# Optimization experiments

Measured on AMD Instinct MI355X. Metric: run time of the kernel, lower is better.

Reference implementation:

```python
import jax, jax.numpy as jnp
import numpy as np
import math

D_MODEL = 512
N_HEADS = 8
WINDOW = 64
LN_EPS = 1e-5


def _layernorm(x, g, b):
    mu = jnp.mean(x, axis=-1, keepdims=True)
    var = jnp.var(x, axis=-1, keepdims=True)
    return (x - mu) * jax.lax.rsqrt(var + LN_EPS) * g + b


def setup_inputs() -> dict:
    key = jax.random.key(0)
    ks = jax.random.split(key, 8)
    B, L, D = 4, 2048, D_MODEL
    s = 0.02
    return {
        "x": jax.random.normal(ks[0], (B, L, D), jnp.float32),
        "wq": jax.random.normal(ks[1], (D, D), jnp.float32) * s,
        "bq": jnp.zeros((D,), jnp.float32),
        "wk": jax.random.normal(ks[2], (D, D), jnp.float32) * s,
        "bk": jnp.zeros((D,), jnp.float32),
        "wv": jax.random.normal(ks[3], (D, D), jnp.float32) * s,
        "bv": jnp.zeros((D,), jnp.float32),
        "wo": jax.random.normal(ks[4], (D, D), jnp.float32) * s,
        "bo": jnp.zeros((D,), jnp.float32),
        "ln1_g": jnp.ones((D,), jnp.float32),
        "ln1_b": jnp.zeros((D,), jnp.float32),
        "w1": jax.random.normal(ks[5], (D, 4 * D), jnp.float32) * s,
        "b1": jnp.zeros((4 * D,), jnp.float32),
        "w2": jax.random.normal(ks[6], (4 * D, D), jnp.float32) * s,
        "b2": jnp.zeros((D,), jnp.float32),
        "ln2_g": jnp.ones((D,), jnp.float32),
        "ln2_b": jnp.zeros((D,), jnp.float32),
    }


def reference(x, wq, bq, wk, bk, wv, bv, wo, bo, ln1_g, ln1_b, w1, b1, w2, b2, ln2_g, ln2_b):
    B, L, D = x.shape
    H, dk = N_HEADS, D // N_HEADS
    # QKV projections -> [B, H, L, dk]
    q = (x @ wq + bq).reshape(B, L, H, dk).transpose(0, 2, 1, 3)
    k = (x @ wk + bk).reshape(B, L, H, dk).transpose(0, 2, 1, 3)
    v = (x @ wv + bv).reshape(B, L, H, dk).transpose(0, 2, 1, 3)
    # dense scores with sliding-window band mask |i-j| <= WINDOW (faithful to original)
    idx = jnp.arange(L)
    band = jnp.abs(idx[:, None] - idx[None, :]) <= WINDOW  # [L, L] bool
    scores = jnp.einsum("bhid,bhjd->bhij", q, k) / math.sqrt(dk)
    scores = jnp.where(band, scores, -jnp.inf)
    attn = jax.nn.softmax(scores, axis=-1)
    out = jnp.einsum("bhij,bhjd->bhid", attn, v)  # [B, H, L, dk]
    out = out.transpose(0, 2, 1, 3).reshape(B, L, D)
    attn_out = out @ wo + bo
    h = _layernorm(x + attn_out, ln1_g, ln1_b)
    ff = jax.nn.relu(h @ w1 + b1) @ w2 + b2
    return _layernorm(h + ff, ln2_g, ln2_b)
```

## Files before the change

### kernel.cpp

```cpp
#include <hip/hip_runtime.h>
#include <hip/hip_bf16.h>

#define D_MODEL 512
#define NHEADS 8
#define DK 64
#define WIN 64
#define SEQ 2048
#define BATCH 4
#define ROWS (BATCH*SEQ)

typedef unsigned short u16;
using bf16x8 = __attribute__((ext_vector_type(8))) short;
using f32x4  = __attribute__((ext_vector_type(4))) float;
using u16x4  = __attribute__((ext_vector_type(4))) unsigned short;

__device__ __forceinline__ u16 f2b(float f) {
  union { float f; unsigned u; } v; v.f = f;
  unsigned r = v.u + 0x7FFFu + ((v.u >> 16) & 1u);
  return (u16)(r >> 16);
}
__device__ __forceinline__ float b2f(u16 h) {
  union { unsigned u; float f; } v; v.u = ((unsigned)h) << 16; return v.f;
}

__device__ __forceinline__ void gload16(const u16* g, u16* l) {
  __builtin_amdgcn_global_load_lds((const __attribute__((address_space(1))) void*)g,
                                   (__attribute__((address_space(3))) void*)l, 16, 0, 0);
}

__global__ __launch_bounds__(256)
void prep_kernel(const float* __restrict__ wq, const float* __restrict__ wk,
                 const float* __restrict__ wv, const float* __restrict__ wo,
                 const float* __restrict__ w1, const float* __restrict__ w2,
                 const float* __restrict__ x,
                 u16* __restrict__ wqt, u16* __restrict__ wkt, u16* __restrict__ wvt,
                 u16* __restrict__ wot, u16* __restrict__ w1t, u16* __restrict__ w2t,
                 u16* __restrict__ xb)
{
  __shared__ u16 T[64][72];
  const int t = blockIdx.x;
  const float* src; u16* dst; int K, N, lt; bool tr = true;
  if (t < 256)      { int m = t >> 6; lt = t & 63;
                      src = m==0?wq:(m==1?wk:(m==2?wv:wo));
                      dst = m==0?wqt:(m==1?wkt:(m==2?wvt:wot));
                      K = 512; N = 512; }
  else if (t < 512) { src = w1; dst = w1t; K = 512;  N = 2048; lt = t-256; }
  else if (t < 768) { src = w2; dst = w2t; K = 2048; N = 512;  lt = t-512; }
  else              { src = x;  dst = xb;  K = 8192; N = 512;  lt = t-768; tr = false; }
  const int ntj = N >> 6;
  const int ti = lt / ntj, tj = lt - ti*ntj;
  const int tid = threadIdx.x;
  const int r = tid >> 2, c0 = (tid & 3) << 4;

  const float* sp = src + (size_t)(ti*64 + r)*N + tj*64 + c0;
  u16 h[16];
  #pragma unroll
  for (int u = 0; u < 4; ++u) {
    float4 v = *(const float4*)(sp + u*4);
    h[u*4+0]=f2b(v.x); h[u*4+1]=f2b(v.y); h[u*4+2]=f2b(v.z); h[u*4+3]=f2b(v.w);
  }
  if (!tr) {
    u16* dp = dst + (size_t)(ti*64 + r)*N + tj*64 + c0;
    *(bf16x8*)(dp)     = *(bf16x8*)&h[0];
    *(bf16x8*)(dp + 8) = *(bf16x8*)&h[8];
    return;
  }
  #pragma unroll
  for (int u = 0; u < 16; ++u) T[r][c0+u] = h[u];
  __syncthreads();
  u16 o[16];
  #pragma unroll
  for (int u = 0; u < 16; ++u) o[u] = T[c0+u][r];
  u16* dp = dst + (size_t)(tj*64 + r)*K + ti*64 + c0;
  *(bf16x8*)(dp)     = *(bf16x8*)&o[0];
  *(bf16x8*)(dp + 8) = *(bf16x8*)&o[8];
}

__device__ __forceinline__ void mainloop_bt(
    const u16* __restrict__ A, const u16* __restrict__ Bt, int K,
    int m0, int n0, int tid, f32x4 (&acc)[4][4], u16* Asl, u16* Bsl)
{
  const int lane = tid & 63, wave = tid >> 6;
  const int wr = wave >> 1, wc = wave & 1;
  const int l15 = lane & 15, lq = lane >> 4;
  const int ar = lane >> 2;
  const int ac = (lane & 3) << 3;

  const u16* ag0 = A  + (size_t)(m0 + wave*32 + ar)*K + ac;
  const u16* bg0 = Bt + (size_t)(n0 + wave*32 + ar)*K + ac;
  u16* const aslw = Asl + wave*1024;
  u16* const bslw = Bsl + wave*1024;

  for (int k0 = 0; k0 < K; k0 += 32) {
    __syncthreads();
    gload16(ag0 + k0,          aslw);
    gload16(ag0 + k0 + 16*K,   aslw + 512);
    gload16(bg0 + k0,          bslw);
    gload16(bg0 + k0 + 16*K,   bslw + 512);
    __syncthreads();

    bf16x8 af[4], bfr[4];
    #pragma unroll
    for (int m = 0; m < 4; ++m)
      af[m] = *(const bf16x8*)(&Asl[(wr*64 + m*16 + l15)*32 + lq*8]);
    #pragma unroll
    for (int n = 0; n < 4; ++n)
      bfr[n] = *(const bf16x8*)(&Bsl[(wc*64 + n*16 + l15)*32 + lq*8]);
    #pragma unroll
    for (int m = 0; m < 4; ++m)
      #pragma unroll
      for (int n = 0; n < 4; ++n)
        acc[m][n] = __builtin_amdgcn_mfma_f32_16x16x32_bf16(af[m], bfr[n], acc[m][n], 0, 0, 0);
  }
}

__global__ __launch_bounds__(256)
void qkv_kernel(const u16* __restrict__ xb,
                const u16* __restrict__ wqt, const float* __restrict__ bq,
                const u16* __restrict__ wkt, const float* __restrict__ bk,
                const u16* __restrict__ wvt, const float* __restrict__ bv,
                u16* __restrict__ qo, u16* __restrict__ ko, u16* __restrict__ vo)
{
  __shared__ __align__(16) u16 Asl[128*32];
  __shared__ __align__(16) u16 Bsl[128*32];
  const u16* Wt; const float* bias; u16* out;
  if (blockIdx.z == 0)      { Wt = wqt; bias = bq; out = qo; }
  else if (blockIdx.z == 1) { Wt = wkt; bias = bk; out = ko; }
  else                      { Wt = wvt; bias = bv; out = vo; }

  const int tid = threadIdx.x;
  const int lane = tid & 63, wave = tid >> 6;
  const int wr = wave >> 1, wc = wave & 1;
  const int l15 = lane & 15, lq = lane >> 4;
  const int m0 = blockIdx.y * 128, n0 = blockIdx.x * 128;

  f32x4 acc[4][4] = {};
  mainloop_bt(xb, Wt, 512, m0, n0, tid, acc, Asl, Bsl);

  #pragma unroll
  for (int n = 0; n < 4; ++n) {
    const int col = n0 + wc*64 + n*16 + l15;
    const float bv2 = bias[col];
    const int h = col >> 6, d = col & 63;
    #pragma unroll
    for (int m = 0; m < 4; ++m)
      #pragma unroll
      for (int j = 0; j < 4; ++j) {
        const int row = m0 + wr*64 + m*16 + lq*4 + j;
        const int b = row >> 11, l = row & (SEQ-1);
        out[(((size_t)(b*NHEADS + h))*SEQ + l)*DK + d] = f2b(acc[m][n][j] + bv2);
      }
  }
}

#define EP_RES  1
#define EP_RELU 2

template<int EP>
__global__ __launch_bounds__(256)
void gemm_bt(const u16* __restrict__ A, const u16* __restrict__ Bt,
             const float* __restrict__ bias, const float* __restrict__ resid,
             void* __restrict__ out_, int K, int N)
{
  __shared__ __align__(16) u16 Asl[128*32];
  __shared__ __align__(16) u16 Bsl[128*32];

  const int tid = threadIdx.x;
  const int lane = tid & 63, wave = tid >> 6;
  const int wr = wave >> 1, wc = wave & 1;
  const int l15 = lane & 15, lq = lane >> 4;
  const int m0 = blockIdx.y * 128, n0 = blockIdx.x * 128;

  f32x4 acc[4][4] = {};
  mainloop_bt(A, Bt, K, m0, n0, tid, acc, Asl, Bsl);

  #pragma unroll
  for (int n = 0; n < 4; ++n) {
    const int col = n0 + wc*64 + n*16 + l15;
    const float bv2 = bias[col];
    #pragma unroll
    for (int m = 0; m < 4; ++m)
      #pragma unroll
      for (int j = 0; j < 4; ++j) {
        const int row = m0 + wr*64 + m*16 + lq*4 + j;
        const size_t o = (size_t)row*N + col;
        float val = acc[m][n][j] + bv2;
        if (EP == EP_RES)  ((float*)out_)[o] = val + resid[o];
        else               ((u16*)out_)[o]   = f2b(fmaxf(val, 0.0f));
      }
  }
}

__global__ __launch_bounds__(256)
void attn_kernel(const u16* __restrict__ q, const u16* __restrict__ k,
                 const u16* __restrict__ v, u16* __restrict__ ctx)
{
  __shared__ __align__(16) u16 Ksl[192*40];
  __shared__ __align__(16) u16 Vt[64*200];
  __shared__ __align__(16) u16 Pl[4][16*200];

  const int bid = blockIdx.x;
  const int t = bid & 31, h = (bid >> 5) & 7, b = bid >> 8;
  const int qs = t*64;
  const int ks0 = max(0, qs - WIN);
  const int ks1 = min(SEQ, qs + 64 + WIN);
  const int span = ks1 - ks0;

  const size_t hoff = ((size_t)(b*NHEADS + h))*SEQ*DK;
  const u16* kh = k + hoff;
  const u16* vh = v + hoff;
  const int tid = threadIdx.x;

  #pragma unroll
  for (int i = 0; i < 6; ++i) {
    int e = tid + i*256;
    int r = e >> 3, c8 = (e & 7) << 3;
    bf16x8 val = {};
    if (r < span) val = *(const bf16x8*)(kh + (size_t)(ks0+r)*DK + c8);
    *(bf16x8*)(&Ksl[r*40 + c8]) = val;
  }
  #pragma unroll
  for (int i = 0; i < 12; ++i) {
    int e = tid + i*256;
    int j = e >> 4, d4 = (e & 15) << 2;
    u16x4 val{};
    if (j < span) val = *(const u16x4*)(vh + (size_t)(ks0+j)*DK + d4);
    #pragma unroll
    for (int u = 0; u < 4; ++u) {
      int d = d4 + u;
      int col = ((((j >> 3) ^ ((d >> 2) & 7)) << 3) | (j & 7));
      Vt[d*200 + col] = (u16)val[u];
    }
  }
  __syncthreads();

  const int wave = tid >> 6, lane = tid & 63;
  const int lq = lane >> 4, l15 = lane & 15;

  const u16* qrow = q + hoff + (size_t)(qs + wave*16 + l15)*DK;
  const bf16x8 qf0 = *(const bf16x8*)(qrow + lq*8);
  const bf16x8 qf1 = *(const bf16x8*)(qrow + 32 + lq*8);

  f32x4 sacc[12];
  #pragma unroll
  for (int m = 0; m < 12; ++m) sacc[m] = f32x4{0.f,0.f,0.f,0.f};
  #pragma unroll
  for (int m = 0; m < 12; ++m) {
    const u16* kr = &Ksl[(m*16 + l15)*40];
    bf16x8 ka0 = *(const bf16x8*)(kr + lq*8);
    bf16x8 ka1 = *(const bf16x8*)(kr + 32 + lq*8);
    sacc[m] = __builtin_amdgcn_mfma_f32_16x16x32_bf16(ka0, qf0, sacc[m], 0, 0, 0);
    sacc[m] = __builtin_amdgcn_mfma_f32_16x16x32_bf16(ka1, qf1, sacc[m], 0, 0, 0);
  }

  const int ig = qs + wave*16 + l15;
  float mx = -3.0e38f;
  #pragma unroll
  for (int m = 0; m < 12; ++m)
    #pragma unroll
    for (int r = 0; r < 4; ++r) {
      int jg = ks0 + m*16 + lq*4 + r;
      bool ok = (jg < ks1) && (jg >= ig - WIN) && (jg <= ig + WIN);
      float sv = ok ? sacc[m][r]*0.125f : -3.0e38f;
      sacc[m][r] = sv;
      mx = fmaxf(mx, sv);
    }
  mx = fmaxf(mx, __shfl_xor(mx, 16));
  mx = fmaxf(mx, __shfl_xor(mx, 32));
  float sum = 0.f;
  #pragma unroll
  for (int m = 0; m < 12; ++m)
    #pragma unroll
    for (int r = 0; r < 4; ++r) {
      float p = __expf(sacc[m][r] - mx);
      sacc[m][r] = p;
      sum += p;
    }
  sum += __shfl_xor(sum, 16);
  sum += __shfl_xor(sum, 32);
  const float inv = 1.0f / sum;

  u16* pw = &Pl[wave][0];
  #pragma unroll
  for (int m = 0; m < 12; ++m) {
    unsigned lo = (unsigned)f2b(sacc[m][0]*inv) | ((unsigned)f2b(sacc[m][1]*inv) << 16);
    unsigned hi = (unsigned)f2b(sacc[m][2]*inv) | ((unsigned)f2b(sacc[m][3]*inv) << 16);
    uint2 pk = make_uint2(lo, hi);
    *(uint2*)(&pw[l15*200 + m*16 + lq*4]) = pk;
  }

  f32x4 oacc[4] = {};
  #pragma unroll
  for (int kst = 0; kst < 6; ++kst) {
    bf16x8 pa = *(const bf16x8*)(&pw[l15*200 + kst*32 + lq*8]);
    #pragma unroll
    for (int n = 0; n < 4; ++n) {
      int d = n*16 + l15;
      int col = (((kst*4 + lq) ^ ((d >> 2) & 7)) << 3);
      bf16x8 vb = *(const bf16x8*)(&Vt[d*200 + col]);
      oacc[n] = __builtin_amdgcn_mfma_f32_16x16x32_bf16(pa, vb, oacc[n], 0, 0, 0);
    }
  }

  #pragma unroll
  for (int n = 0; n < 4; ++n)
    #pragma unroll
    for (int r = 0; r < 4; ++r) {
      int i = wave*16 + lq*4 + r;
      ctx[((size_t)b*SEQ + qs + i)*D_MODEL + h*DK + n*16 + l15] = f2b(oacc[n][r]);
    }
}

template<bool WB16>
__global__ __launch_bounds__(256)
void ln_kernel(const float* __restrict__ in, const float* __restrict__ g,
               const float* __restrict__ bb, float* __restrict__ out,
               u16* __restrict__ out16)
{
  const int row = blockIdx.x*4 + (threadIdx.x >> 6);
  const int lane = threadIdx.x & 63;
  const float* p = in + (size_t)row*D_MODEL + lane*8;
  float4 v0 = *(const float4*)(p);
  float4 v1 = *(const float4*)(p + 4);
  float s  = v0.x+v0.y+v0.z+v0.w + v1.x+v1.y+v1.z+v1.w;
  float sq = v0.x*v0.x+v0.y*v0.y+v0.z*v0.z+v0.w*v0.w
           + v1.x*v1.x+v1.y*v1.y+v1.z*v1.z+v1.w*v1.w;
  #pragma unroll
  for (int off = 32; off; off >>= 1) { s += __shfl_xor(s, off); sq += __shfl_xor(sq, off); }
  const float mean = s * (1.0f/D_MODEL);
  const float var  = sq * (1.0f/D_MODEL) - mean*mean;
  const float rstd = rsqrtf(var + 1e-5f);
  float4 g0 = *(const float4*)(g + lane*8);
  float4 g1 = *(const float4*)(g + lane*8 + 4);
  float4 b0 = *(const float4*)(bb + lane*8);
  float4 b1 = *(const float4*)(bb + lane*8 + 4);
  float4 o0, o1;
  o0.x = (v0.x-mean)*rstd*g0.x + b0.x;
  o0.y = (v0.y-mean)*rstd*g0.y + b0.y;
  o0.z = (v0.z-mean)*rstd*g0.z + b0.z;
  o0.w = (v0.w-mean)*rstd*g0.w + b0.w;
  o1.x = (v1.x-mean)*rstd*g1.x + b1.x;
  o1.y = (v1.y-mean)*rstd*g1.y + b1.y;
  o1.z = (v1.z-mean)*rstd*g1.z + b1.z;
  o1.w = (v1.w-mean)*rstd*g1.w + b1.w;
  float* qo = out + (size_t)row*D_MODEL + lane*8;
  *(float4*)(qo)     = o0;
  *(float4*)(qo + 4) = o1;
  if (WB16) {
    u16 hh[8];
    hh[0]=f2b(o0.x); hh[1]=f2b(o0.y); hh[2]=f2b(o0.z); hh[3]=f2b(o0.w);
    hh[4]=f2b(o1.x); hh[5]=f2b(o1.y); hh[6]=f2b(o1.z); hh[7]=f2b(o1.w);
    *(bf16x8*)(out16 + (size_t)row*D_MODEL + lane*8) = *(bf16x8*)&hh[0];
  }
}

extern "C" void kernel_launch(void* const* d_in, const int* in_sizes, int n_in,
                              void* d_out, int out_size, void* d_ws, size_t ws_size,
                              hipStream_t stream)
{
  (void)in_sizes; (void)n_in; (void)out_size; (void)ws_size;
  const float* x  = (const float*)d_in[0];
  const float* wq = (const float*)d_in[1];
  const float* bq = (const float*)d_in[2];
  const float* wk = (const float*)d_in[3];
  const float* bk = (const float*)d_in[4];
  const float* wv = (const float*)d_in[5];
  const float* bv = (const float*)d_in[6];
  const float* wo = (const float*)d_in[7];
  const float* bo = (const float*)d_in[8];
  const float* g1 = (const float*)d_in[9];
  const float* be1= (const float*)d_in[10];
  const float* w1 = (const float*)d_in[11];
  const float* b1 = (const float*)d_in[12];
  const float* w2 = (const float*)d_in[13];
  const float* b2 = (const float*)d_in[14];
  const float* g2 = (const float*)d_in[15];
  const float* be2= (const float*)d_in[16];

  const size_t RD = (size_t)ROWS * D_MODEL;
  u16* W = (u16*)d_ws;
  u16*   xb   = W;
  u16*   qb   = W + RD;
  u16*   kb   = W + 2*RD;
  u16*   vb   = W + 3*RD;
  u16*   ctxb = W + 4*RD;
  u16*   hb16 = W + 5*RD;
  float* hbuf = (float*)(W + 6*RD);
  u16*   wqt  = W + 8*RD;
  u16*   wkt  = wqt + 512*512;
  u16*   wvt  = wkt + 512*512;
  u16*   wot  = wvt + 512*512;
  u16*   w1t  = wot + 512*512;
  u16*   w2t  = w1t + 512*2048;
  u16*   ff1  = qb;
  float* pre  = (float*)d_out;
  float* outp = (float*)d_out;

  dim3 blk(256);
  prep_kernel<<<dim3(1792), blk, 0, stream>>>(wq, wk, wv, wo, w1, w2, x,
                                              wqt, wkt, wvt, wot, w1t, w2t, xb);
  qkv_kernel<<<dim3(4,64,3), blk, 0, stream>>>(xb, wqt, bq, wkt, bk, wvt, bv, qb, kb, vb);
  attn_kernel<<<dim3(BATCH*NHEADS*32), blk, 0, stream>>>(qb, kb, vb, ctxb);
  gemm_bt<EP_RES><<<dim3(4,64), blk, 0, stream>>>(ctxb, wot, bo, x, pre, 512, 512);
  ln_kernel<true><<<dim3(ROWS/4), blk, 0, stream>>>(pre, g1, be1, hbuf, hb16);
  gemm_bt<EP_RELU><<<dim3(16,64), blk, 0, stream>>>(hb16, w1t, b1, nullptr, ff1, 512, 2048);
  gemm_bt<EP_RES><<<dim3(4,64), blk, 0, stream>>>(ff1, w2t, b2, hbuf, pre, 2048, 512);
  ln_kernel<false><<<dim3(ROWS/4), blk, 0, stream>>>(pre, g2, be2, outp, nullptr);
}
```

Baseline: 268.3 us.

## Double-buffer LDS in GEMM mainloop and swap grid axes for M-major launch

The GEMM mainloop now uses two LDS buffers. The next K-tile's global-to-LDS loads are issued before the current tile's MFMAs, and only one barrier per iteration remains instead of two. Separately, grid x now indexes M tiles and y indexes N tiles, which changes block scheduling order and therefore L2 reuse of weight and activation tiles. LDS use per block doubles to 32KB, which could reduce occupancy.

```diff
diff --git a/kernel.cpp b/kernel.cpp
--- a/kernel.cpp
+++ b/kernel.cpp
@@ -78,7 +78,8 @@
 
 __device__ __forceinline__ void mainloop_bt(
     const u16* __restrict__ A, const u16* __restrict__ Bt, int K,
-    int m0, int n0, int tid, f32x4 (&acc)[4][4], u16* Asl, u16* Bsl)
+    int m0, int n0, int tid, f32x4 (&acc)[4][4],
+    u16 (*Asl)[128*32], u16 (*Bsl)[128*32])
 {
   const int lane = tid & 63, wave = tid >> 6;
   const int wr = wave >> 1, wc = wave & 1;
@@ -88,30 +89,41 @@
 
   const u16* ag0 = A  + (size_t)(m0 + wave*32 + ar)*K + ac;
   const u16* bg0 = Bt + (size_t)(n0 + wave*32 + ar)*K + ac;
-  u16* const aslw = Asl + wave*1024;
-  u16* const bslw = Bsl + wave*1024;
-
-  for (int k0 = 0; k0 < K; k0 += 32) {
-    __syncthreads();
-    gload16(ag0 + k0,          aslw);
-    gload16(ag0 + k0 + 16*K,   aslw + 512);
-    gload16(bg0 + k0,          bslw);
-    gload16(bg0 + k0 + 16*K,   bslw + 512);
-    __syncthreads();
-
+
+  auto stage = [&](int buf, int k0) {
+    u16* aslw = &Asl[buf][wave*1024];
+    u16* bslw = &Bsl[buf][wave*1024];
+    gload16(ag0 + k0,        aslw);
+    gload16(ag0 + k0 + 16*K, aslw + 512);
+    gload16(bg0 + k0,        bslw);
+    gload16(bg0 + k0 + 16*K, bslw + 512);
+  };
+  auto compute = [&](int buf) {
     bf16x8 af[4], bfr[4];
     #pragma unroll
     for (int m = 0; m < 4; ++m)
-      af[m] = *(const bf16x8*)(&Asl[(wr*64 + m*16 + l15)*32 + lq*8]);
+      af[m] = *(const bf16x8*)(&Asl[buf][(wr*64 + m*16 + l15)*32 + lq*8]);
     #pragma unroll
     for (int n = 0; n < 4; ++n)
-      bfr[n] = *(const bf16x8*)(&Bsl[(wc*64 + n*16 + l15)*32 + lq*8]);
+      bfr[n] = *(const bf16x8*)(&Bsl[buf][(wc*64 + n*16 + l15)*32 + lq*8]);
     #pragma unroll
     for (int m = 0; m < 4; ++m)
       #pragma unroll
       for (int n = 0; n < 4; ++n)
         acc[m][n] = __builtin_amdgcn_mfma_f32_16x16x32_bf16(af[m], bfr[n], acc[m][n], 0, 0, 0);
-  }
+  };
+
+  stage(0, 0);
+  __syncthreads();
+  int cur = 0;
+  const int nt = K >> 5;
+  for (int t = 0; t < nt - 1; ++t) {
+    stage(cur ^ 1, (t + 1) << 5);
+    compute(cur);
+    __syncthreads();
+    cur ^= 1;
+  }
+  compute(cur);
 }
 
 __global__ __launch_bounds__(256)
@@ -121,8 +133,8 @@
                 const u16* __restrict__ wvt, const float* __restrict__ bv,
                 u16* __restrict__ qo, u16* __restrict__ ko, u16* __restrict__ vo)
 {
-  __shared__ __align__(16) u16 Asl[128*32];
-  __shared__ __align__(16) u16 Bsl[128*32];
+  __shared__ __align__(16) u16 Asl[2][128*32];
+  __shared__ __align__(16) u16 Bsl[2][128*32];
   const u16* Wt; const float* bias; u16* out;
   if (blockIdx.z == 0)      { Wt = wqt; bias = bq; out = qo; }
   else if (blockIdx.z == 1) { Wt = wkt; bias = bk; out = ko; }
@@ -132,7 +144,7 @@
   const int lane = tid & 63, wave = tid >> 6;
   const int wr = wave >> 1, wc = wave & 1;
   const int l15 = lane & 15, lq = lane >> 4;
-  const int m0 = blockIdx.y * 128, n0 = blockIdx.x * 128;
+  const int m0 = blockIdx.x * 128, n0 = blockIdx.y * 128;
 
   f32x4 acc[4][4] = {};
   mainloop_bt(xb, Wt, 512, m0, n0, tid, acc, Asl, Bsl);
@@ -162,14 +174,14 @@
              const float* __restrict__ bias, const float* __restrict__ resid,
              void* __restrict__ out_, int K, int N)
 {
-  __shared__ __align__(16) u16 Asl[128*32];
-  __shared__ __align__(16) u16 Bsl[128*32];
+  __shared__ __align__(16) u16 Asl[2][128*32];
+  __shared__ __align__(16) u16 Bsl[2][128*32];
 
   const int tid = threadIdx.x;
   const int lane = tid & 63, wave = tid >> 6;
   const int wr = wave >> 1, wc = wave & 1;
   const int l15 = lane & 15, lq = lane >> 4;
-  const int m0 = blockIdx.y * 128, n0 = blockIdx.x * 128;
+  const int m0 = blockIdx.x * 128, n0 = blockIdx.y * 128;
 
   f32x4 acc[4][4] = {};
   mainloop_bt(A, Bt, K, m0, n0, tid, acc, Asl, Bsl);
@@ -399,11 +411,11 @@
   dim3 blk(256);
   prep_kernel<<<dim3(1792), blk, 0, stream>>>(wq, wk, wv, wo, w1, w2, x,
                                               wqt, wkt, wvt, wot, w1t, w2t, xb);
-  qkv_kernel<<<dim3(4,64,3), blk, 0, stream>>>(xb, wqt, bq, wkt, bk, wvt, bv, qb, kb, vb);
+  qkv_kernel<<<dim3(64,4,3), blk, 0, stream>>>(xb, wqt, bq, wkt, bk, wvt, bv, qb, kb, vb);
   attn_kernel<<<dim3(BATCH*NHEADS*32), blk, 0, stream>>>(qb, kb, vb, ctxb);
-  gemm_bt<EP_RES><<<dim3(4,64), blk, 0, stream>>>(ctxb, wot, bo, x, pre, 512, 512);
+  gemm_bt<EP_RES><<<dim3(64,4), blk, 0, stream>>>(ctxb, wot, bo, x, pre, 512, 512);
   ln_kernel<true><<<dim3(ROWS/4), blk, 0, stream>>>(pre, g1, be1, hbuf, hb16);
-  gemm_bt<EP_RELU><<<dim3(16,64), blk, 0, stream>>>(hb16, w1t, b1, nullptr, ff1, 512, 2048);
-  gemm_bt<EP_RES><<<dim3(4,64), blk, 0, stream>>>(ff1, w2t, b2, hbuf, pre, 2048, 512);
+  gemm_bt<EP_RELU><<<dim3(64,16), blk, 0, stream>>>(hb16, w1t, b1, nullptr, ff1, 512, 2048);
+  gemm_bt<EP_RES><<<dim3(64,4), blk, 0, stream>>>(ff1, w2t, b2, hbuf, pre, 2048, 512);
   ln_kernel<false><<<dim3(ROWS/4), blk, 0, stream>>>(pre, g2, be2, outp, nullptr);
 }
```

After: 262.7 us. 1.02x faster.
